# Kernel tuning notes

Hardware: AMD Instinct MI355X
Metric: run time of the kernel (lower is better)

The kernel has to match this reference:

```python
import jax, jax.numpy as jnp
import numpy as np

B, T, D_IN, D_PROJ, D_OUT, MEM = 8, 2048, 1024, 1024, 1024, 40


def setup_inputs() -> dict:
    key = jax.random.key(0)
    k1, k2, k3, k4 = jax.random.split(key, 4)
    x = jax.random.normal(k1, (B, T, D_IN), dtype=jnp.float32)
    # xavier-uniform-style params
    lim1 = np.sqrt(6.0 / (D_IN + D_PROJ))
    lim2 = np.sqrt(6.0 / (D_PROJ + D_OUT))
    limm = np.sqrt(6.0 / (MEM + 1 + D_PROJ))
    W1 = jax.random.uniform(k2, (D_IN, D_PROJ), minval=-lim1, maxval=lim1, dtype=jnp.float32)
    W2 = jax.random.uniform(k3, (D_PROJ, D_OUT), minval=-lim2, maxval=lim2, dtype=jnp.float32)
    mw = jax.random.uniform(k4, (MEM + 1, D_PROJ), minval=-limm, maxval=limm, dtype=jnp.float32)
    mw = mw.at[0].set(0.0)  # row 0 zeroed at init (still trainable in the original)
    bias1 = jnp.ones((D_PROJ,), dtype=jnp.float32)
    bias2 = jnp.ones((D_OUT,), dtype=jnp.float32)
    return {"input_data": x, "W1": W1, "bias1": bias1, "W2": W2, "bias2": bias2,
            "memory_weights": mw}


def _fsmn_memory(p, memory_weights):
    # p: [B, T, D], memory_weights: [M+1, D]
    # Original gather index: mm[i,j] = i-j+1 for 0<=i-j<=M-1, else 0.
    # => out[b,i,d] = sum_{l=0}^{M-1} w[l+1,d]*p[b,i-l,d]
    #              + w[0,d] * (sum_j p[b,j,d] - sum_{l=0}^{M-1} p[b,i-l,d])
    M = memory_weights.shape[0] - 1
    b, t, d = p.shape
    # causal depthwise conv: taps w[1:] with lag l -> kernel position M-1-l
    rhs = memory_weights[1:][::-1].T[:, None, :]           # [D, 1, M]
    lhs = jnp.pad(p.transpose(0, 2, 1), ((0, 0), (0, 0), (M - 1, 0)))  # [B, D, T+M-1]
    band = jax.lax.conv_general_dilated(
        lhs, rhs, window_strides=(1,), padding='VALID',
        feature_group_count=d,
        dimension_numbers=('NCH', 'OIH', 'NCH')).transpose(0, 2, 1)    # [B, T, D]
    # in-band running sum via cumsum difference
    cs = jnp.cumsum(p, axis=1)                              # [B, T, D]
    band_sum = cs - jnp.pad(cs, ((0, 0), (M, 0), (0, 0)))[:, :t]
    total = cs[:, -1:]                                      # [B, 1, D]
    return band + memory_weights[0] * (total - band_sum)


def reference(input_data, W1, bias1, W2, bias2, memory_weights):
    p = jnp.matmul(input_data, W1) + bias1                  # [B, T, D_PROJ]
    p = _fsmn_memory(p, memory_weights)
    return jnp.matmul(p, W2) + bias2                        # [B, T, D_OUT]
```

## Files before the change

kernel.cpp:

```cpp
#include <hip/hip_runtime.h>

typedef __attribute__((ext_vector_type(8))) short bf16x8;
typedef __attribute__((ext_vector_type(4))) float f32x4;

typedef const __attribute__((address_space(1))) void* as1cv;
typedef __attribute__((address_space(3))) void* as3v;

__device__ __forceinline__ unsigned short f2bf(float f) {
    union { float f; unsigned u; } x; x.f = f;
    unsigned r = x.u + 0x7FFFu + ((x.u >> 16) & 1u);
    return (unsigned short)(r >> 16);
}
__device__ __forceinline__ float bf2f(unsigned short u) {
    union { unsigned u; float f; } x; x.u = ((unsigned)u) << 16; return x.f;
}

__global__ void k_cvt_bf16(const float* __restrict__ in, unsigned short* __restrict__ out, long n) {
    long i = (long)blockIdx.x * blockDim.x + threadIdx.x;
    long stride = (long)gridDim.x * blockDim.x;
    long n4 = n >> 2;
    for (long j = i; j < n4; j += stride) {
        float4 v = ((const float4*)in)[j];
        ushort4 o;
        o.x = f2bf(v.x); o.y = f2bf(v.y); o.z = f2bf(v.z); o.w = f2bf(v.w);
        ((ushort4*)out)[j] = o;
    }
}

__global__ void k_transpose_bf16(const float* __restrict__ W, unsigned short* __restrict__ Wt,
                                 int rows, int cols) {
    __shared__ float tile[64][65];
    int r0 = blockIdx.y * 64, c0 = blockIdx.x * 64;
    #pragma unroll
    for (int i = 0; i < 16; ++i) {
        int idx = threadIdx.x + i * 256;
        int r = idx >> 6, c = idx & 63;
        tile[r][c] = W[(long)(r0 + r) * cols + (c0 + c)];
    }
    __syncthreads();
    #pragma unroll
    for (int i = 0; i < 16; ++i) {
        int idx = threadIdx.x + i * 256;
        int r = idx >> 6, c = idx & 63;
        Wt[(long)(c0 + r) * rows + (r0 + c)] = f2bf(tile[c][r]);
    }
}

template<int OUT_BF16>
__global__ __launch_bounds__(512, 2) void k_gemm256(
    const unsigned short* __restrict__ A,
    const unsigned short* __restrict__ Bt,
    const float* __restrict__ bias,
    void* __restrict__ C,
    int M, int N, int K)
{
    __shared__ unsigned short lds[2][4][8192];
    const int tid  = threadIdx.x;
    const int lane = tid & 63;
    const int w    = tid >> 6;
    const int wm   = w >> 2;
    const int wn   = w & 3;

    const int nwg = gridDim.x;
    const int cpx = nwg >> 3;
    const int wg  = (blockIdx.x & 7) * cpx + (blockIdx.x >> 3);
    const int nblks = N >> 8;
    const int mblk = wg / nblks, nblk = wg % nblks;
    const long m0 = (long)mblk << 8, n0 = (long)nblk << 8;

    const int segRow  = lane >> 3;
    const long segColE = (long)(((lane & 7) ^ segRow) << 3);

    const int rr = lane & 15, cc = lane >> 4;
    const int smask = (rr & 7) << 4;
    const int colSwz0 = (((cc * 16) ^ smask) >> 1);
    const int colSwz1 = (((64 + cc * 16) ^ smask) >> 1);

    auto stage = [&](int buf, int slot, const unsigned short* src, long rowBase, int kt) {
        #pragma unroll
        for (int g = 0; g < 2; ++g) {
            const int s = w + g * 8;
            const unsigned short* gp = src + (rowBase + s * 8 + segRow) * (long)K
                                           + (long)kt * 64 + segColE;
            __builtin_amdgcn_global_load_lds((as1cv)gp,
                (as3v)(&lds[buf][slot][s * 512 + lane * 8]), 16, 0, 0);
        }
    };

    f32x4 acc[8][4];
    #pragma unroll
    for (int i = 0; i < 8; ++i)
        #pragma unroll
        for (int j = 0; j < 4; ++j)
            acc[i][j] = (f32x4){0.f, 0.f, 0.f, 0.f};

    bf16x8 bfrag[4][2];
    const int bRowBase = (wn & 1) * 64;
    const int NK = K >> 6;
    const int ITERS = K >> 7;

#define VM4   asm volatile("s_waitcnt vmcnt(4)" ::: "memory")
#define PHASE(BUF, Q, STAGES, VMW) do {                                              \
    bf16x8 af0_0, af0_1, af1_0, af1_1;                                               \
    { const unsigned short* Ah = &lds[BUF][wm][0];                                   \
      af0_0 = *(const bf16x8*)(Ah + ((Q)*32 + rr) * 64 + colSwz0);                   \
      af0_1 = *(const bf16x8*)(Ah + ((Q)*32 + rr) * 64 + colSwz1);                   \
      af1_0 = *(const bf16x8*)(Ah + ((Q)*32 + 16 + rr) * 64 + colSwz0);              \
      af1_1 = *(const bf16x8*)(Ah + ((Q)*32 + 16 + rr) * 64 + colSwz1); }            \
    if ((Q) == 0) { const unsigned short* Bh = &lds[BUF][2 + (wn >> 1)][0];          \
      _Pragma("unroll")                                                              \
      for (int nj = 0; nj < 4; ++nj) {                                               \
        bfrag[nj][0] = *(const bf16x8*)(Bh + (bRowBase + nj*16 + rr) * 64 + colSwz0);\
        bfrag[nj][1] = *(const bf16x8*)(Bh + (bRowBase + nj*16 + rr) * 64 + colSwz1);\
      } }                                                                            \
    STAGES;                                                                          \
    VMW;                                                                             \
    __builtin_amdgcn_s_barrier();                                                    \
    asm volatile("s_waitcnt lgkmcnt(0)" ::: "memory");                               \
    __builtin_amdgcn_sched_barrier(0);                                               \
    __builtin_amdgcn_s_setprio(1);                                                   \
    _Pragma("unroll")                                                                \
    for (int nj = 0; nj < 4; ++nj) {                                                 \
      acc[2*(Q)][nj]   = __builtin_amdgcn_mfma_f32_16x16x32_bf16(af0_0, bfrag[nj][0], acc[2*(Q)][nj],   0,0,0); \
      acc[2*(Q)][nj]   = __builtin_amdgcn_mfma_f32_16x16x32_bf16(af0_1, bfrag[nj][1], acc[2*(Q)][nj],   0,0,0); \
      acc[2*(Q)+1][nj] = __builtin_amdgcn_mfma_f32_16x16x32_bf16(af1_0, bfrag[nj][0], acc[2*(Q)+1][nj], 0,0,0); \
      acc[2*(Q)+1][nj] = __builtin_amdgcn_mfma_f32_16x16x32_bf16(af1_1, bfrag[nj][1], acc[2*(Q)+1][nj], 0,0,0); \
    }                                                                                \
    __builtin_amdgcn_s_setprio(0);                                                   \
    __builtin_amdgcn_s_barrier();                                                    \
} while (0)

    stage(0, 0, A,  m0,       0);
    stage(0, 1, A,  m0 + 128, 0);
    stage(0, 2, Bt, n0,       0);
    stage(0, 3, Bt, n0 + 128, 0);
    stage(1, 2, Bt, n0,       1);
    stage(1, 3, Bt, n0 + 128, 1);
    VM4;
    __builtin_amdgcn_s_barrier();

    for (int it = 0; it < ITERS; ++it) {
        const int kt1 = 2 * it + 1;
        int kt2 = 2 * it + 2; if (kt2 >= NK) kt2 = 0;
        int kt3 = 2 * it + 3; if (kt3 >= NK) kt3 = 1;

        PHASE(0, 0, stage(1, 0, A,  m0,       kt1), );
        PHASE(0, 1, stage(1, 1, A,  m0 + 128, kt1), );
        PHASE(0, 2, { stage(0, 2, Bt, n0, kt2); stage(0, 3, Bt, n0 + 128, kt2); }, );
        PHASE(0, 3, , VM4);
        PHASE(1, 0, stage(0, 0, A,  m0,       kt2), );
        PHASE(1, 1, stage(0, 1, A,  m0 + 128, kt2), );
        PHASE(1, 2, { stage(1, 2, Bt, n0, kt3); stage(1, 3, Bt, n0 + 128, kt3); }, );
        PHASE(1, 3, , VM4);
    }
#undef PHASE
#undef VM4

    #pragma unroll
    for (int mi = 0; mi < 8; ++mi) {
        const long rowb = m0 + wm * 128 + mi * 16 + cc * 4;
        #pragma unroll
        for (int nj = 0; nj < 4; ++nj) {
            const long col = n0 + wn * 64 + nj * 16 + rr;
            const float bv = bias[col];
            #pragma unroll
            for (int jj = 0; jj < 4; ++jj) {
                const float v = acc[mi][nj][jj] + bv;
                if (OUT_BF16) ((unsigned short*)C)[(rowb + jj) * N + col] = f2bf(v);
                else          ((float*)C)[(rowb + jj) * N + col] = v;
            }
        }
    }
}

__global__ void k_colsum(const unsigned short* __restrict__ p, float* __restrict__ total, int T) {
    const int b = blockIdx.y;
    const int t0 = blockIdx.x * 64;
    const int tid = threadIdx.x;
    float s0 = 0.f, s1 = 0.f, s2 = 0.f, s3 = 0.f;
    const unsigned short* base = p + ((long)b * T + t0) * 1024 + tid * 4;
    for (int t = 0; t < 64; ++t) {
        ushort4 v = *(const ushort4*)(base + (long)t * 1024);
        s0 += bf2f(v.x); s1 += bf2f(v.y); s2 += bf2f(v.z); s3 += bf2f(v.w);
    }
    float* tp = total + b * 1024 + tid * 4;
    atomicAdd(tp + 0, s0); atomicAdd(tp + 1, s1);
    atomicAdd(tp + 2, s2); atomicAdd(tp + 3, s3);
}

#define SP_STRIDE 73
__global__ __launch_bounds__(256, 2) void k_fsmn(
    const unsigned short* __restrict__ p,
    const float* __restrict__ mw,
    const float* __restrict__ total,
    unsigned short* __restrict__ p2,
    int T)
{
    __shared__ float spT[64 * SP_STRIDE];
    const int b  = blockIdx.z;
    const int t0 = blockIdx.y * 32;
    const int d0 = blockIdx.x * 64;
    const int tid = threadIdx.x;

    for (int i = 0; i < 18; ++i) {
        int idx = tid + i * 256;
        if (idx < 71 * 64) {
            int c = idx >> 6, dcol = idx & 63;
            int t = t0 + c - 39;
            float v = 0.f;
            if (t >= 0) v = bf2f(p[((long)b * T + t) * 1024 + d0 + dcol]);
            spT[dcol * SP_STRIDE + c] = v;
        }
    }
    __syncthreads();

    const int lane = tid & 63, tg = tid >> 6;
    const int d  = d0 + lane;
    const int tb = t0 + tg * 8;
    const float* wp = spT + lane * SP_STRIDE + tg * 8;

    float w[47];
    #pragma unroll
    for (int j = 40; j < 47; ++j) w[j] = wp[j];
    float S_hi = ((w[40] + w[41]) + (w[42] + w[43])) + ((w[44] + w[45]) + w[46]);
    float S_all = S_hi;

    float acc[8] = {0,0,0,0,0,0,0,0};
    #pragma unroll
    for (int lag = 0; lag < 40; ++lag) {
        const int jn = 39 - lag;
        w[jn] = wp[jn];
        S_all += w[jn];
        const float m = mw[(1 + lag) * 1024 + d];
        #pragma unroll
        for (int t = 0; t < 8; ++t)
            acc[t] = fmaf(m, w[t + jn], acc[t]);
    }

    float accw[8];
    accw[0] = S_all - S_hi;
    #pragma unroll
    for (int t = 1; t < 8; ++t) accw[t] = accw[t - 1] + w[t + 39] - w[t - 1];

    const float m0v = mw[d];
    const float tot = total[b * 1024 + d];
    unsigned short* ob = p2 + ((long)b * T + tb) * 1024 + d;
    #pragma unroll
    for (int t = 0; t < 8; ++t)
        ob[(long)t * 1024] = f2bf(acc[t] + m0v * (tot - accw[t]));
}

extern "C" void kernel_launch(void* const* d_in, const int* in_sizes, int n_in,
                              void* d_out, int out_size, void* d_ws, size_t ws_size,
                              hipStream_t stream) {
    const float* x  = (const float*)d_in[0];
    const float* W1 = (const float*)d_in[1];
    const float* b1 = (const float*)d_in[2];
    const float* W2 = (const float*)d_in[3];
    const float* b2 = (const float*)d_in[4];
    const float* mw = (const float*)d_in[5];
    float* out = (float*)d_out;

    const int B = 8, T = 2048;
    const long M = (long)B * T;
    const int N = 1024, K = 1024;

    char* ws = (char*)d_ws;
    unsigned short* x_bf   = (unsigned short*)(ws);
    unsigned short* W1t    = (unsigned short*)(ws + 33554432L);
    unsigned short* W2t    = (unsigned short*)(ws + 35651584L);
    unsigned short* p_bf   = (unsigned short*)(ws + 37748736L);
    float*          totals = (float*)(ws + 71303168L);
    unsigned short* p2_bf  = x_bf;

    k_cvt_bf16<<<2048, 256, 0, stream>>>(x, x_bf, M * 1024);

    dim3 tgrid(16, 16);
    k_transpose_bf16<<<tgrid, 256, 0, stream>>>(W1, W1t, K, N);
    k_transpose_bf16<<<tgrid, 256, 0, stream>>>(W2, W2t, K, N);

    k_gemm256<1><<<dim3((int)((M / 256) * (N / 256))), 512, 0, stream>>>(
        x_bf, W1t, b1, (void*)p_bf, (int)M, N, K);

    hipMemsetAsync(totals, 0, B * 1024 * sizeof(float), stream);
    k_colsum<<<dim3(T / 64, B), 256, 0, stream>>>(p_bf, totals, T);

    k_fsmn<<<dim3(1024 / 64, T / 32, B), 256, 0, stream>>>(p_bf, mw, totals, p2_bf, T);

    k_gemm256<0><<<dim3((int)((M / 256) * (N / 256))), 512, 0, stream>>>(
        p2_bf, W2t, b2, (void*)out, (int)M, N, K);
}
```

Baseline: 150.1 us.

## Enlarge FSMN time tile and stage memory weights and bf16 input in LDS

The FSMN memory kernel now covers 128 time steps per block instead of 32, which cuts the halo re-read overhead from 39/32 to 39/128 rows. The bf16 input stays bf16 in shared memory and is loaded with 16-byte vectors. Memory weights are staged once per block in LDS and kept in registers. Each thread handles 16 outputs per pass over two passes. Register pressure is much higher (40 weights, 55 window values, 16 accumulators) and the grid has fewer blocks.

```diff
diff --git a/kernel.cpp b/kernel.cpp
--- a/kernel.cpp
+++ b/kernel.cpp
@@ -2,6 +2,7 @@
 
 typedef __attribute__((ext_vector_type(8))) short bf16x8;
 typedef __attribute__((ext_vector_type(4))) float f32x4;
+typedef __attribute__((ext_vector_type(8))) unsigned short u16x8;
 
 typedef const __attribute__((address_space(1))) void* as1cv;
 typedef __attribute__((address_space(3))) void* as3v;
@@ -188,7 +189,7 @@
     atomicAdd(tp + 2, s2); atomicAdd(tp + 3, s3);
 }
 
-#define SP_STRIDE 73
+#define FS_ROWS 167
 __global__ __launch_bounds__(256, 2) void k_fsmn(
     const unsigned short* __restrict__ p,
     const float* __restrict__ mw,
@@ -196,58 +197,76 @@
     unsigned short* __restrict__ p2,
     int T)
 {
-    __shared__ float spT[64 * SP_STRIDE];
+    __shared__ unsigned short sp[FS_ROWS][64];
+    __shared__ float smw[41][64];
     const int b  = blockIdx.z;
-    const int t0 = blockIdx.y * 32;
+    const int t0 = blockIdx.y * 128;
     const int d0 = blockIdx.x * 64;
     const int tid = threadIdx.x;
 
-    for (int i = 0; i < 18; ++i) {
-        int idx = tid + i * 256;
-        if (idx < 71 * 64) {
-            int c = idx >> 6, dcol = idx & 63;
-            int t = t0 + c - 39;
-            float v = 0.f;
-            if (t >= 0) v = bf2f(p[((long)b * T + t) * 1024 + d0 + dcol]);
-            spT[dcol * SP_STRIDE + c] = v;
+    for (int idx = tid; idx < 41 * 64; idx += 256) {
+        int r = idx >> 6, c = idx & 63;
+        smw[r][c] = mw[r * 1024 + d0 + c];
+    }
+    {
+        const int row0 = tid >> 3;
+        const int col8 = (tid & 7) * 8;
+        #pragma unroll
+        for (int i = 0; i < 6; ++i) {
+            const int row = row0 + i * 32;
+            if (row < FS_ROWS) {
+                const int t = t0 + row - 39;
+                u16x8 v = {0, 0, 0, 0, 0, 0, 0, 0};
+                if (t >= 0)
+                    v = *(const u16x8*)(p + ((long)b * T + t) * 1024 + d0 + col8);
+                *(u16x8*)(&sp[row][col8]) = v;
+            }
         }
     }
     __syncthreads();
 
-    const int lane = tid & 63, tg = tid >> 6;
-    const int d  = d0 + lane;
-    const int tb = t0 + tg * 8;
-    const float* wp = spT + lane * SP_STRIDE + tg * 8;
-
-    float w[47];
-    #pragma unroll
-    for (int j = 40; j < 47; ++j) w[j] = wp[j];
-    float S_hi = ((w[40] + w[41]) + (w[42] + w[43])) + ((w[44] + w[45]) + w[46]);
-    float S_all = S_hi;
-
-    float acc[8] = {0,0,0,0,0,0,0,0};
-    #pragma unroll
-    for (int lag = 0; lag < 40; ++lag) {
-        const int jn = 39 - lag;
-        w[jn] = wp[jn];
-        S_all += w[jn];
-        const float m = mw[(1 + lag) * 1024 + d];
-        #pragma unroll
-        for (int t = 0; t < 8; ++t)
-            acc[t] = fmaf(m, w[t + jn], acc[t]);
-    }
-
-    float accw[8];
-    accw[0] = S_all - S_hi;
-    #pragma unroll
-    for (int t = 1; t < 8; ++t) accw[t] = accw[t - 1] + w[t + 39] - w[t - 1];
-
-    const float m0v = mw[d];
+    const int lane = tid & 63, wv = tid >> 6;
+    const int d = d0 + lane;
+
+    float m[40];
+    #pragma unroll
+    for (int l = 0; l < 40; ++l) m[l] = smw[l + 1][lane];
+    const float m0v = smw[0][lane];
     const float tot = total[b * 1024 + d];
-    unsigned short* ob = p2 + ((long)b * T + tb) * 1024 + d;
-    #pragma unroll
-    for (int t = 0; t < 8; ++t)
-        ob[(long)t * 1024] = f2bf(acc[t] + m0v * (tot - accw[t]));
+
+    #pragma unroll
+    for (int pass = 0; pass < 2; ++pass) {
+        const int obase = wv * 32 + pass * 16;
+        float w[55];
+        #pragma unroll
+        for (int j = 0; j < 55; ++j) w[j] = bf2f(sp[obase + j][lane]);
+
+        float acc[16];
+        #pragma unroll
+        for (int s = 0; s < 16; ++s) acc[s] = 0.f;
+        #pragma unroll
+        for (int lag = 0; lag < 40; ++lag) {
+            const float mm = m[lag];
+            #pragma unroll
+            for (int s = 0; s < 16; ++s)
+                acc[s] = fmaf(mm, w[s + 39 - lag], acc[s]);
+        }
+
+        float accw[16];
+        {
+            float S = 0.f;
+            #pragma unroll
+            for (int j = 0; j < 40; ++j) S += w[j];
+            accw[0] = S;
+            #pragma unroll
+            for (int s = 1; s < 16; ++s) accw[s] = accw[s - 1] + w[s + 39] - w[s - 1];
+        }
+
+        unsigned short* ob = p2 + ((long)b * T + t0 + obase) * 1024 + d;
+        #pragma unroll
+        for (int s = 0; s < 16; ++s)
+            ob[(long)s * 1024] = f2bf(acc[s] + m0v * (tot - accw[s]));
+    }
 }
 
 extern "C" void kernel_launch(void* const* d_in, const int* in_sizes, int n_in,
@@ -285,7 +304,7 @@
     hipMemsetAsync(totals, 0, B * 1024 * sizeof(float), stream);
     k_colsum<<<dim3(T / 64, B), 256, 0, stream>>>(p_bf, totals, T);
 
-    k_fsmn<<<dim3(1024 / 64, T / 32, B), 256, 0, stream>>>(p_bf, mw, totals, p2_bf, T);
+    k_fsmn<<<dim3(1024 / 64, T / 128, B), 256, 0, stream>>>(p_bf, mw, totals, p2_bf, T);
 
     k_gemm256<0><<<dim3((int)((M / 256) * (N / 256))), 512, 0, stream>>>(
         p2_bf, W2t, b2, (void*)out, (int)M, N, K);
```

Result: faster. 137.7 us (-8.3%).
